# Optimization experiments

Measured on AMD Instinct MI355X. Metric: run time of the kernel, lower is better.

The kernel has to match this reference:

```python
import jax, jax.numpy as jnp
import numpy as np

EMBED = 1024
HEADS = 16
HEAD_DIM = EMBED // HEADS
EPS = 1e-8


def setup_inputs() -> dict:
    key = jax.random.key(0)
    ks = jax.random.split(key, 10)
    s = 1.0 / np.sqrt(EMBED)
    return {
        "hidden_input": jax.random.normal(ks[0], (4, 2048, EMBED), dtype=jnp.float32),
        "Wq": jax.random.uniform(ks[1], (EMBED, EMBED), jnp.float32, -s, s),
        "bq": jax.random.uniform(ks[2], (EMBED,), jnp.float32, -s, s),
        "Wk": jax.random.uniform(ks[3], (EMBED, EMBED), jnp.float32, -s, s),
        "bk": jax.random.uniform(ks[4], (EMBED,), jnp.float32, -s, s),
        "Wv": jax.random.uniform(ks[5], (EMBED, EMBED), jnp.float32, -s, s),
        "bv": jax.random.uniform(ks[6], (EMBED,), jnp.float32, -s, s),
        "Wp": jax.random.uniform(ks[7], (EMBED, EMBED), jnp.float32, -s, s),
        "bp": jax.random.uniform(ks[8], (EMBED,), jnp.float32, -s, s),
        "gamma": jnp.ones((EMBED,), jnp.float32),
        "beta": jnp.zeros((EMBED,), jnp.float32),
    }


def reference(hidden_input, Wq, bq, Wk, bk, Wv, bv, Wp, bp, gamma, beta):
    n, l, e = hidden_input.shape
    h, d = HEADS, HEAD_DIM

    def split_heads(x):  # [n, l, e] -> [n, h, l, d]
        return x.reshape(n, l, h, d).transpose(0, 2, 1, 3)

    q = split_heads(hidden_input @ Wq + bq)
    k = split_heads(hidden_input @ Wk + bk)
    v = split_heads(hidden_input @ Wv + bv)

    scores = jnp.einsum("nhqd,nhkd->nhqk", q, k) / jnp.sqrt(jnp.float32(d))
    attn = jax.nn.softmax(scores, axis=-1)
    ctx = jnp.einsum("nhqk,nhkd->nhqd", attn, v)
    ctx = ctx.transpose(0, 2, 1, 3).reshape(n, l, e)

    out = ctx @ Wp + bp
    x = out + hidden_input
    mu = jnp.mean(x, axis=-1, keepdims=True)
    var = jnp.mean(jnp.square(x - mu), axis=-1, keepdims=True)
    return (x - mu) / jnp.sqrt(var + EPS) * gamma + beta
```

## Files before the change

kernel.cpp:

```cpp
#include <hip/hip_runtime.h>

#define EMBED 1024
#define SEQ   2048
#define BATCH 4
#define HEADS 16

typedef __attribute__((ext_vector_type(8))) short short8;
typedef __attribute__((ext_vector_type(4))) float floatx4;

#define MFMA16(a, b, c) __builtin_amdgcn_mfma_f32_16x16x32_bf16((a), (b), (c), 0, 0, 0)
#define ATT_SCALE (0.125f * 1.44269504088896340736f)

static __device__ __forceinline__ unsigned short f2bf(float f) {
  union { float f; unsigned int u; } v; v.f = f;
  unsigned int u = v.u;
  u += 0x7fffu + ((u >> 16) & 1u);
  return (unsigned short)(u >> 16);
}

static __device__ __forceinline__ void async16(const unsigned short* g, unsigned short* l) {
  __builtin_amdgcn_global_load_lds(
      (const __attribute__((address_space(1))) void*)g,
      (__attribute__((address_space(3))) void*)l, 16, 0, 0);
}

__global__ __launch_bounds__(256) void k_prep(const float* __restrict__ hid,
                                              unsigned short* __restrict__ hidA,
                                              const float* __restrict__ Wq, const float* __restrict__ Wk,
                                              const float* __restrict__ Wv, const float* __restrict__ Wp,
                                              unsigned short* __restrict__ WT) {
  __shared__ unsigned short tile[64][65];
  const int bid = blockIdx.x, tid = threadIdx.x;
  if (bid < 4096) {
    int i = bid * 256 + tid;
    const float4* s = (const float4*)hid;
    float4 a = s[i * 2], b = s[i * 2 + 1];
    uint4 o;
    o.x = (unsigned)f2bf(a.x) | ((unsigned)f2bf(a.y) << 16);
    o.y = (unsigned)f2bf(a.z) | ((unsigned)f2bf(a.w) << 16);
    o.z = (unsigned)f2bf(b.x) | ((unsigned)f2bf(b.y) << 16);
    o.w = (unsigned)f2bf(b.z) | ((unsigned)f2bf(b.w) << 16);
    ((uint4*)hidA)[i] = o;
    return;
  }
  const int idx = bid - 4096;
  const int z = idx >> 8, rem = idx & 255;
  const float* src = (z == 0) ? Wq : (z == 1) ? Wk : (z == 2) ? Wv : Wp;
  unsigned short* dst = WT + (size_t)z * EMBED * EMBED;
  const int k0 = (rem & 15) * 64, n0 = (rem >> 4) * 64;
  for (int i = tid; i < 4096; i += 256) {
    int r = i >> 6, c = i & 63;
    tile[c][r] = f2bf(src[(size_t)(k0 + r) * EMBED + n0 + c]);
  }
  __syncthreads();
  for (int i = tid; i < 4096; i += 256) {
    int r = i >> 6, c = i & 63;
    dst[(size_t)(n0 + r) * EMBED + k0 + c] = tile[r][c];
  }
}

__global__ __launch_bounds__(256) void k_gemm_qkv(const unsigned short* __restrict__ A,
                                                  const unsigned short* __restrict__ BT,
                                                  const float* __restrict__ bq,
                                                  const float* __restrict__ bk,
                                                  const float* __restrict__ bv,
                                                  unsigned short* __restrict__ C) {
  __shared__ unsigned short Als[128 * 64];
  __shared__ unsigned short Bls[128 * 64];
  const int tid = threadIdx.x;
  const int m0 = blockIdx.x * 128, n0 = blockIdx.y * 128;
  const int w = tid >> 6, lane = tid & 63, l16 = lane & 15, quad = lane >> 4;
  const int l7 = l16 & 7;
  const int wrow = (w >> 1) * 64, wcol = (w & 1) * 64;

  floatx4 acc[4][4];
#pragma unroll
  for (int i = 0; i < 4; ++i)
#pragma unroll
    for (int j = 0; j < 4; ++j) acc[i][j] = {0.f, 0.f, 0.f, 0.f};

  const int srow = tid >> 3;
  const int scol = (((tid & 7) ^ (srow & 7)) * 8);
  const unsigned short* Ap = A + (size_t)(m0 + srow) * EMBED + scol;
  const unsigned short* Bp = BT + (size_t)(n0 + srow) * EMBED + scol;

  int ab[2], bb[2];
#pragma unroll
  for (int kc = 0; kc < 2; ++kc) {
    ab[kc] = (wrow + l16) * 64 + (((4 * kc + quad) ^ l7) << 3);
    bb[kc] = (wcol + l16) * 64 + (((4 * kc + quad) ^ l7) << 3);
  }

  for (int kt = 0; kt < 16; ++kt) {
    const int k0 = kt * 64;
#pragma unroll
    for (int i = 0; i < 4; ++i)
      async16(Ap + k0 + (size_t)i * 32 * EMBED, Als + i * 2048 + tid * 8);
#pragma unroll
    for (int i = 0; i < 4; ++i)
      async16(Bp + k0 + (size_t)i * 32 * EMBED, Bls + i * 2048 + tid * 8);
    __syncthreads();
    short8 af[4][2], bf[4][2];
#pragma unroll
    for (int mt = 0; mt < 4; ++mt)
#pragma unroll
      for (int kc = 0; kc < 2; ++kc)
        af[mt][kc] = *(const short8*)(Als + ab[kc] + mt * 1024);
#pragma unroll
    for (int nt = 0; nt < 4; ++nt)
#pragma unroll
      for (int kc = 0; kc < 2; ++kc)
        bf[nt][kc] = *(const short8*)(Bls + bb[kc] + nt * 1024);
#pragma unroll
    for (int kc = 0; kc < 2; ++kc)
#pragma unroll
      for (int mt = 0; mt < 4; ++mt)
#pragma unroll
        for (int nt = 0; nt < 4; ++nt)
          acc[mt][nt] = MFMA16(af[mt][kc], bf[nt][kc], acc[mt][nt]);
    __syncthreads();
  }

  const float* bsel = (n0 < 1024) ? bq : (n0 < 2048 ? bk : bv);
  const float scl = (n0 < 1024) ? ATT_SCALE : 1.0f;
  const int nb = n0 & 1023;
  float bias[4];
#pragma unroll
  for (int nt = 0; nt < 4; ++nt) bias[nt] = bsel[nb + wcol + nt * 16 + l16];
#pragma unroll
  for (int mt = 0; mt < 4; ++mt)
#pragma unroll
    for (int r = 0; r < 4; ++r) {
      int gm = m0 + wrow + mt * 16 + quad * 4 + r;
      size_t base = (size_t)gm * 3072 + n0 + wcol;
#pragma unroll
      for (int nt = 0; nt < 4; ++nt)
        C[base + nt * 16 + l16] = f2bf((acc[mt][nt][r] + bias[nt]) * scl);
    }
}

__global__ __launch_bounds__(256) void k_vt(const unsigned short* __restrict__ QKV,
                                            unsigned short* __restrict__ VT) {
  int lt = blockIdx.x;
  int bh = blockIdx.y;
  int b = bh >> 4, h = bh & 15;
  int l0 = lt * 64;
  __shared__ unsigned short tile[64][65];
  const unsigned short* src = QKV + (size_t)(b * SEQ) * 3072 + 2048 + h * 64;
  unsigned short* dst = VT + (size_t)bh * 64 * SEQ;
  int tid = threadIdx.x;
  for (int i = tid; i < 4096; i += 256) {
    int r = i >> 6, c = i & 63;
    tile[c][r] = src[(size_t)(l0 + r) * 3072 + c];
  }
  __syncthreads();
  for (int i = tid; i < 4096; i += 256) {
    int r = i >> 6, c = i & 63;
    int cp = (c & 15) * 4 + (c >> 4);
    dst[(size_t)r * SEQ + l0 + cp] = tile[r][c];
  }
}

__global__ __launch_bounds__(256, 2) void k_attn(const unsigned short* __restrict__ QKV,
                                                 const unsigned short* __restrict__ VT,
                                                 unsigned short* __restrict__ CTX) {
  const int bh = blockIdx.x, qt = blockIdx.y;
  const int b = bh >> 4, h = bh & 15;
  const int tid = threadIdx.x;
  const int w = tid >> 6, lane = tid & 63, l16 = lane & 15, quad = lane >> 4;

  __shared__ unsigned short Kls[64 * 64];
  __shared__ unsigned short Vls[64 * 64];
  __shared__ unsigned short Pls[4][64 * 64];

  const unsigned short* Qb = QKV + (size_t)(b * SEQ + qt * 256 + w * 64) * 3072 + h * 64;
  const unsigned short* Kb = QKV + (size_t)(b * SEQ) * 3072 + 1024 + h * 64;
  const unsigned short* Vb = VT + (size_t)bh * 64 * SEQ;
  unsigned short* Pw = Pls[w];

  int pwb[4];
#pragma unroll
  for (int r = 0; r < 4; ++r)
    pwb[r] = (quad * 4 + r) * 64 + ((((l16 >> 1) + quad * 4 + r) & 7) << 3) + ((l16 & 1) << 2);
  int prb[2];
#pragma unroll
  for (int kc = 0; kc < 2; ++kc)
    prb[kc] = l16 * 64 + (((kc * 4 + quad + l16) & 7) << 3);

  short8 qf[4][2];
#pragma unroll
  for (int mt = 0; mt < 4; ++mt)
#pragma unroll
    for (int kc = 0; kc < 2; ++kc)
      qf[mt][kc] = *(const short8*)(Qb + (size_t)(mt * 16 + l16) * 3072 + kc * 32 + quad * 8);

  floatx4 o[4][4];
  float rs[4][4];
#pragma unroll
  for (int mt = 0; mt < 4; ++mt)
#pragma unroll
    for (int nt = 0; nt < 4; ++nt) { o[mt][nt] = {0.f, 0.f, 0.f, 0.f}; rs[mt][nt] = 0.f; }

  const int srow = tid >> 3;
  const int scol = (((tid & 7) ^ (srow & 7)) * 8);

  for (int kt = 0; kt < 32; ++kt) {
    const int kv0 = kt * 64;
    async16(Kb + (size_t)(kv0 + srow) * 3072 + scol, Kls + tid * 8);
    async16(Kb + (size_t)(kv0 + 32 + srow) * 3072 + scol, Kls + 2048 + tid * 8);
    async16(Vb + (size_t)srow * SEQ + kv0 + scol, Vls + tid * 8);
    async16(Vb + (size_t)(32 + srow) * SEQ + kv0 + scol, Vls + 2048 + tid * 8);
    __syncthreads();

    short8 kf[4][2];
#pragma unroll
    for (int nt = 0; nt < 4; ++nt)
#pragma unroll
      for (int kc = 0; kc < 2; ++kc) {
        int row = nt * 16 + l16;
        kf[nt][kc] = *(const short8*)(Kls + row * 64 + (((kc * 4 + quad) ^ (row & 7)) * 8));
      }

#pragma unroll
    for (int mt = 0; mt < 4; ++mt) {
      floatx4 s[4];
#pragma unroll
      for (int nt = 0; nt < 4; ++nt) {
        floatx4 z = {0.f, 0.f, 0.f, 0.f};
        z = MFMA16(qf[mt][0], kf[nt][0], z);
        s[nt] = MFMA16(qf[mt][1], kf[nt][1], z);
      }
#pragma unroll
      for (int r = 0; r < 4; ++r) {
        union { float f; unsigned u; } c0, c1, c2, c3;
        c0.f = __builtin_amdgcn_exp2f(s[0][r]);
        c1.f = __builtin_amdgcn_exp2f(s[1][r]);
        c2.f = __builtin_amdgcn_exp2f(s[2][r]);
        c3.f = __builtin_amdgcn_exp2f(s[3][r]);
        rs[mt][r] += (c0.f + c1.f) + (c2.f + c3.f);
        uint2 pk;
        pk.x = __builtin_amdgcn_perm(c1.u, c0.u, 0x07060302);
        pk.y = __builtin_amdgcn_perm(c3.u, c2.u, 0x07060302);
        *(uint2*)(Pw + pwb[r] + mt * 1024) = pk;
      }
    }

    __asm__ volatile("s_waitcnt lgkmcnt(0)" ::: "memory");

    short8 vf[4][2];
#pragma unroll
    for (int nt = 0; nt < 4; ++nt)
#pragma unroll
      for (int kc = 0; kc < 2; ++kc) {
        int row = nt * 16 + l16;
        vf[nt][kc] = *(const short8*)(Vls + row * 64 + (((kc * 4 + quad) ^ (row & 7)) * 8));
      }
#pragma unroll
    for (int kc = 0; kc < 2; ++kc)
#pragma unroll
      for (int mt = 0; mt < 4; ++mt) {
        short8 pf = *(const short8*)(Pw + prb[kc] + mt * 1024);
#pragma unroll
        for (int nt = 0; nt < 4; ++nt)
          o[mt][nt] = MFMA16(pf, vf[nt][kc], o[mt][nt]);
      }
    __syncthreads();
  }

#pragma unroll
  for (int mt = 0; mt < 4; ++mt)
#pragma unroll
    for (int r = 0; r < 4; ++r) {
      float v = rs[mt][r];
#pragma unroll
      for (int off = 1; off < 16; off <<= 1) v += __shfl_xor(v, off);
      rs[mt][r] = 1.f / v;
    }

#pragma unroll
  for (int mt = 0; mt < 4; ++mt)
#pragma unroll
    for (int r = 0; r < 4; ++r) {
      int gq = b * SEQ + qt * 256 + w * 64 + mt * 16 + quad * 4 + r;
      float inv = rs[mt][r];
      size_t base = (size_t)gq * EMBED + h * 64;
#pragma unroll
      for (int nt = 0; nt < 4; ++nt)
        CTX[base + nt * 16 + l16] = f2bf(o[mt][nt][r] * inv);
    }
}

__global__ __launch_bounds__(256) void k_gemm_proj(const unsigned short* __restrict__ A,
                                                   const unsigned short* __restrict__ BT,
                                                   const float* __restrict__ bp,
                                                   const float* __restrict__ hid,
                                                   float* __restrict__ X) {
  __shared__ unsigned short Als[128 * 64];
  __shared__ unsigned short Bls[128 * 64];
  const int tid = threadIdx.x;
  const int m0 = blockIdx.x * 128, n0 = blockIdx.y * 128;
  const int w = tid >> 6, lane = tid & 63, l16 = lane & 15, quad = lane >> 4;
  const int l7 = l16 & 7;
  const int wrow = (w >> 1) * 64, wcol = (w & 1) * 64;

  floatx4 acc[4][4];
#pragma unroll
  for (int i = 0; i < 4; ++i)
#pragma unroll
    for (int j = 0; j < 4; ++j) acc[i][j] = {0.f, 0.f, 0.f, 0.f};

  const int srow = tid >> 3;
  const int scol = (((tid & 7) ^ (srow & 7)) * 8);
  const unsigned short* Ap = A + (size_t)(m0 + srow) * EMBED + scol;
  const unsigned short* Bp = BT + (size_t)(n0 + srow) * EMBED + scol;

  int ab[2], bb[2];
#pragma unroll
  for (int kc = 0; kc < 2; ++kc) {
    ab[kc] = (wrow + l16) * 64 + (((4 * kc + quad) ^ l7) << 3);
    bb[kc] = (wcol + l16) * 64 + (((4 * kc + quad) ^ l7) << 3);
  }

  for (int kt = 0; kt < 16; ++kt) {
    const int k0 = kt * 64;
#pragma unroll
    for (int i = 0; i < 4; ++i)
      async16(Ap + k0 + (size_t)i * 32 * EMBED, Als + i * 2048 + tid * 8);
#pragma unroll
    for (int i = 0; i < 4; ++i)
      async16(Bp + k0 + (size_t)i * 32 * EMBED, Bls + i * 2048 + tid * 8);
    __syncthreads();
    short8 af[4][2], bf[4][2];
#pragma unroll
    for (int mt = 0; mt < 4; ++mt)
#pragma unroll
      for (int kc = 0; kc < 2; ++kc)
        af[mt][kc] = *(const short8*)(Als + ab[kc] + mt * 1024);
#pragma unroll
    for (int nt = 0; nt < 4; ++nt)
#pragma unroll
      for (int kc = 0; kc < 2; ++kc)
        bf[nt][kc] = *(const short8*)(Bls + bb[kc] + nt * 1024);
#pragma unroll
    for (int kc = 0; kc < 2; ++kc)
#pragma unroll
      for (int mt = 0; mt < 4; ++mt)
#pragma unroll
        for (int nt = 0; nt < 4; ++nt)
          acc[mt][nt] = MFMA16(af[mt][kc], bf[nt][kc], acc[mt][nt]);
    __syncthreads();
  }

  float bias[4];
#pragma unroll
  for (int nt = 0; nt < 4; ++nt) bias[nt] = bp[n0 + wcol + nt * 16 + l16];
#pragma unroll
  for (int mt = 0; mt < 4; ++mt)
#pragma unroll
    for (int r = 0; r < 4; ++r) {
      int gm = m0 + wrow + mt * 16 + quad * 4 + r;
      size_t base = (size_t)gm * EMBED + n0 + wcol;
#pragma unroll
      for (int nt = 0; nt < 4; ++nt) {
        size_t idx = base + nt * 16 + l16;
        X[idx] = acc[mt][nt][r] + bias[nt] + hid[idx];
      }
    }
}

__global__ __launch_bounds__(256) void k_ln(float* __restrict__ x,
                                            const float* __restrict__ gamma,
                                            const float* __restrict__ beta) {
  int row = blockIdx.x, tid = threadIdx.x;
  float4* rp = (float4*)(x + (size_t)row * EMBED);
  float4 v = rp[tid];
  float s = v.x + v.y + v.z + v.w;
  float q = v.x * v.x + v.y * v.y + v.z * v.z + v.w * v.w;
#pragma unroll
  for (int off = 1; off < 64; off <<= 1) {
    s += __shfl_xor(s, off);
    q += __shfl_xor(q, off);
  }
  __shared__ float ss[4], sq[4];
  int w = tid >> 6;
  if ((tid & 63) == 0) { ss[w] = s; sq[w] = q; }
  __syncthreads();
  s = ss[0] + ss[1] + ss[2] + ss[3];
  q = sq[0] + sq[1] + sq[2] + sq[3];
  float mean = s * (1.f / 1024.f);
  float var = q * (1.f / 1024.f) - mean * mean;
  float rstd = rsqrtf(var + 1e-8f);
  float4 g = ((const float4*)gamma)[tid];
  float4 be = ((const float4*)beta)[tid];
  v.x = (v.x - mean) * rstd * g.x + be.x;
  v.y = (v.y - mean) * rstd * g.y + be.y;
  v.z = (v.z - mean) * rstd * g.z + be.z;
  v.w = (v.w - mean) * rstd * g.w + be.w;
  rp[tid] = v;
}

extern "C" void kernel_launch(void* const* d_in, const int* in_sizes, int n_in,
                              void* d_out, int out_size, void* d_ws, size_t ws_size,
                              hipStream_t stream) {
  const float* hid   = (const float*)d_in[0];
  const float* Wq    = (const float*)d_in[1];
  const float* bq    = (const float*)d_in[2];
  const float* Wk    = (const float*)d_in[3];
  const float* bk    = (const float*)d_in[4];
  const float* Wv    = (const float*)d_in[5];
  const float* bv    = (const float*)d_in[6];
  const float* Wp    = (const float*)d_in[7];
  const float* bp    = (const float*)d_in[8];
  const float* gamma = (const float*)d_in[9];
  const float* beta  = (const float*)d_in[10];
  float* out = (float*)d_out;

  char* ws = (char*)d_ws;
  unsigned short* hidA = (unsigned short*)ws;
  unsigned short* WT   = (unsigned short*)(ws + (size_t)(16 << 20));
  unsigned short* QKV  = (unsigned short*)(ws + (size_t)(24 << 20));
  unsigned short* VT   = (unsigned short*)(ws + (size_t)(72 << 20));
  unsigned short* CTX  = (unsigned short*)(ws + (size_t)(88 << 20));

  k_prep<<<5120, 256, 0, stream>>>(hid, hidA, Wq, Wk, Wv, Wp, WT);
  k_gemm_qkv<<<dim3(64, 24), 256, 0, stream>>>(hidA, WT, bq, bk, bv, QKV);
  k_vt<<<dim3(32, 64), 256, 0, stream>>>(QKV, VT);
  k_attn<<<dim3(64, 8), 256, 0, stream>>>(QKV, VT, CTX);
  k_gemm_proj<<<dim3(64, 8), 256, 0, stream>>>(CTX, WT + (size_t)3 * EMBED * EMBED, bp, hid, out);
  k_ln<<<8192, 256, 0, stream>>>(out, gamma, beta);
}
```

Before: 296.4 us.

## Double-buffer K/V tiles in attention loop and raise MFMA wave priority

```diff
diff --git a/kernel.cpp b/kernel.cpp
--- a/kernel.cpp
+++ b/kernel.cpp
@@ -169,8 +169,8 @@
   const int tid = threadIdx.x;
   const int w = tid >> 6, lane = tid & 63, l16 = lane & 15, quad = lane >> 4;
 
-  __shared__ unsigned short Kls[64 * 64];
-  __shared__ unsigned short Vls[64 * 64];
+  __shared__ unsigned short Kls[2][64 * 64];
+  __shared__ unsigned short Vls[2][64 * 64];
   __shared__ unsigned short Pls[4][64 * 64];
 
   const unsigned short* Qb = QKV + (size_t)(b * SEQ + qt * 256 + w * 64) * 3072 + h * 64;
@@ -204,13 +204,25 @@
   const int srow = tid >> 3;
   const int scol = (((tid & 7) ^ (srow & 7)) * 8);
 
+  async16(Kb + (size_t)srow * 3072 + scol, Kls[0] + tid * 8);
+  async16(Kb + (size_t)(32 + srow) * 3072 + scol, Kls[0] + 2048 + tid * 8);
+  async16(Vb + (size_t)srow * SEQ + scol, Vls[0] + tid * 8);
+  async16(Vb + (size_t)(32 + srow) * SEQ + scol, Vls[0] + 2048 + tid * 8);
+  __syncthreads();
+
+  int cur = 0;
   for (int kt = 0; kt < 32; ++kt) {
-    const int kv0 = kt * 64;
-    async16(Kb + (size_t)(kv0 + srow) * 3072 + scol, Kls + tid * 8);
-    async16(Kb + (size_t)(kv0 + 32 + srow) * 3072 + scol, Kls + 2048 + tid * 8);
-    async16(Vb + (size_t)srow * SEQ + kv0 + scol, Vls + tid * 8);
-    async16(Vb + (size_t)(32 + srow) * SEQ + kv0 + scol, Vls + 2048 + tid * 8);
-    __syncthreads();
+    if (kt < 31) {
+      const int kn = (kt + 1) * 64;
+      unsigned short* Kd = Kls[cur ^ 1];
+      unsigned short* Vd = Vls[cur ^ 1];
+      async16(Kb + (size_t)(kn + srow) * 3072 + scol, Kd + tid * 8);
+      async16(Kb + (size_t)(kn + 32 + srow) * 3072 + scol, Kd + 2048 + tid * 8);
+      async16(Vb + (size_t)srow * SEQ + kn + scol, Vd + tid * 8);
+      async16(Vb + (size_t)(32 + srow) * SEQ + kn + scol, Vd + 2048 + tid * 8);
+    }
+    const unsigned short* Kc = Kls[cur];
+    const unsigned short* Vc = Vls[cur];
 
     short8 kf[4][2];
 #pragma unroll
@@ -218,18 +230,20 @@
 #pragma unroll
       for (int kc = 0; kc < 2; ++kc) {
         int row = nt * 16 + l16;
-        kf[nt][kc] = *(const short8*)(Kls + row * 64 + (((kc * 4 + quad) ^ (row & 7)) * 8));
+        kf[nt][kc] = *(const short8*)(Kc + row * 64 + (((kc * 4 + quad) ^ (row & 7)) * 8));
       }
 
 #pragma unroll
     for (int mt = 0; mt < 4; ++mt) {
       floatx4 s[4];
+      __builtin_amdgcn_s_setprio(1);
 #pragma unroll
       for (int nt = 0; nt < 4; ++nt) {
         floatx4 z = {0.f, 0.f, 0.f, 0.f};
         z = MFMA16(qf[mt][0], kf[nt][0], z);
         s[nt] = MFMA16(qf[mt][1], kf[nt][1], z);
       }
+      __builtin_amdgcn_s_setprio(0);
 #pragma unroll
       for (int r = 0; r < 4; ++r) {
         union { float f; unsigned u; } c0, c1, c2, c3;
@@ -253,8 +267,9 @@
 #pragma unroll
       for (int kc = 0; kc < 2; ++kc) {
         int row = nt * 16 + l16;
-        vf[nt][kc] = *(const short8*)(Vls + row * 64 + (((kc * 4 + quad) ^ (row & 7)) * 8));
-      }
+        vf[nt][kc] = *(const short8*)(Vc + row * 64 + (((kc * 4 + quad) ^ (row & 7)) * 8));
+      }
+    __builtin_amdgcn_s_setprio(1);
 #pragma unroll
     for (int kc = 0; kc < 2; ++kc)
 #pragma unroll
@@ -264,7 +279,10 @@
         for (int nt = 0; nt < 4; ++nt)
           o[mt][nt] = MFMA16(pf, vf[nt][kc], o[mt][nt]);
       }
+    __builtin_amdgcn_s_setprio(0);
+
     __syncthreads();
+    cur ^= 1;
   }
 
 #pragma unroll
```

Result: faster. 287.6 us (-3.0%).
